# Optimization experiments

Hardware: AMD Instinct MI355X
Metric: run time of the kernel (lower is better)

The kernel has to match this reference:

```python
import jax, jax.numpy as jnp
import numpy as np

K = 49        # k_neighbors
EPS = 1e-5    # BatchNorm2d eps


def setup_inputs() -> dict:
    key = jax.random.key(0)
    ks = jax.random.split(key, 2)
    B, C, M, O = 64, 64, 32, 128
    X = jax.random.normal(ks[0], (B, C, M, M), dtype=jnp.float32)
    # conv1x1 weight (kaiming fan_out) flattened to (O, C); bias init 0
    W = jax.random.normal(ks[1], (O, C), dtype=jnp.float32) * (2.0 / O) ** 0.5
    b = jnp.zeros((O,), jnp.float32)
    gamma = jnp.ones((O,), jnp.float32)
    beta = jnp.zeros((O,), jnp.float32)
    run_mean = jnp.zeros((O,), jnp.float32)
    run_var = jnp.ones((O,), jnp.float32)
    return dict(X=X, W=W, b=b, gamma=gamma, beta=beta,
                run_mean=run_mean, run_var=run_var)


def _knn_aggregate(x):
    """x: (N, C) node features -> D^{-1/2} A D^{-1/2} x for the kNN graph."""
    N = x.shape[0]
    sq = jnp.sum(x * x, axis=1)
    d2 = sq[:, None] + sq[None, :] - 2.0 * (x @ x.T)
    dist = jnp.sqrt(jnp.maximum(d2, 0.0))              # torch.cdist (p=2)
    i = jnp.arange(N)
    dist = dist.at[i, i].set(jnp.inf)                  # fill_diagonal_(inf)
    _, knn = jax.lax.top_k(-dist, K)                   # (N, K) nearest indices
    # topk indices are distinct -> every row degree == K, and the column
    # normalizer uses the col node's row degree (also K), so
    # D^{-1/2} A D^{-1/2} x == mean of gathered neighbors.
    nb = x[knn]                                        # (N, K, C) gather
    return nb.sum(axis=1) / K


def reference(X, W, b, gamma, beta, run_mean, run_var):
    B, C, M, _ = X.shape
    N = M * M
    x = X.reshape(B, C, N).transpose(0, 2, 1)          # (B, N, C) nodes
    Z = jax.vmap(_knn_aggregate)(x)                    # (B, N, C) sparse GCN agg
    # 1x1 conv over the (M, M) grid == per-node linear map
    Fg = jnp.einsum('oc,bnc->bon', W, Z) + b[None, :, None]   # (B, O, N)
    Fg = jax.nn.relu(Fg)
    # BatchNorm2d with running stats (eval mode); Dropout2d is identity in eval
    inv = jax.lax.rsqrt(run_var + EPS)
    Fg = gamma[None, :, None] * (Fg - run_mean[None, :, None]) * inv[None, :, None] + beta[None, :, None]
    return Fg.mean(axis=2)                             # AdaptiveAvgPool2d(1) -> (B, O)
```

## Files before the change

### kernel.cpp

```cpp
#include <hip/hip_runtime.h>
#include <stdint.h>

#define BATCH 64
#define CDIM  64
#define NPTS  1024
#define ODIM  128
#define KNN   49
#define KNNP  52
#define BNEPS 1e-5f

typedef __attribute__((ext_vector_type(8))) short bf16x8;
typedef __attribute__((ext_vector_type(4))) float f32x4;

#define O_XF   0
#define SZ_XF  (BATCH*64*2*64*8*4)
#define O_SQ   (O_XF + SZ_XF)
#define SZ_SQ  (BATCH*NPTS*4)
#define O_KNN  (O_SQ + SZ_SQ)
#define SZ_KNN (BATCH*NPTS*KNNP*4)
#define O_Z    (O_KNN + SZ_KNN)
#define SZ_Z   (BATCH*NPTS*CDIM*4)
#define WS_NEED ((size_t)(O_Z + SZ_Z))

__global__ void gcn_init(const float* __restrict__ gamma, const float* __restrict__ beta,
                         const float* __restrict__ rmean, const float* __restrict__ rvar,
                         float* __restrict__ out) {
    int i = blockIdx.x * 256 + threadIdx.x;
    if (i < BATCH * ODIM) {
        int o = i & (ODIM - 1);
        out[i] = beta[o] - gamma[o] * rmean[o] * rsqrtf(rvar[o] + BNEPS);
    }
}

__global__ __launch_bounds__(256) void k0_split(const float* __restrict__ X,
                                                uint32_t* __restrict__ XF,
                                                float* __restrict__ sq) {
    const int b    = blockIdx.x >> 4;
    const int t16  = (blockIdx.x & 15) * 4 + (threadIdx.x >> 6);
    const int lane = threadIdx.x & 63;
    const int n    = t16 * 16 + (lane & 15);
    const int cg   = lane >> 4;
    const float* Xb = X + (size_t)b * CDIM * NPTS;
    float s = 0.f;
    for (int ks = 0; ks < 2; ks++) {
        uint32_t hi[4], lo[4];
#pragma unroll
        for (int dj = 0; dj < 4; dj++) {
            uint32_t hw[2], lw[2];
#pragma unroll
            for (int e = 0; e < 2; e++) {
                int c = ks * 32 + cg * 8 + dj * 2 + e;
                float x = Xb[(size_t)c * NPTS + n];
                s += x * x;
                uint32_t u  = __float_as_uint(x);
                uint32_t hr = (u + 0x7FFFu + ((u >> 16) & 1u)) >> 16;
                float    hf = __uint_as_float(hr << 16);
                uint32_t ul = __float_as_uint(x - hf);
                uint32_t lr = (ul + 0x7FFFu + ((ul >> 16) & 1u)) >> 16;
                hw[e] = hr; lw[e] = lr;
            }
            hi[dj] = hw[0] | (hw[1] << 16);
            lo[dj] = lw[0] | (lw[1] << 16);
        }
        size_t entry = ((size_t)(b * 64 + t16) * 2 + ks) * 64 + lane;
        uint32_t* p = XF + entry * 8;
        *(uint4*)p       = make_uint4(hi[0], hi[1], hi[2], hi[3]);
        *(uint4*)(p + 4) = make_uint4(lo[0], lo[1], lo[2], lo[3]);
    }
    s += __shfl_xor(s, 16, 64);
    s += __shfl_xor(s, 32, 64);
    if (lane < 16) sq[b * NPTS + n] = s;
}

__global__ __launch_bounds__(512, 6) void k1_gram_select(const uint32_t* __restrict__ XF,
                                                         const float* __restrict__ sq,
                                                         int* __restrict__ knn) {
    __shared__ uint32_t s_pk[8 * 1024];
    const int b    = blockIdx.x >> 6;
    const int rt   = blockIdx.x & 63;
    const int wave = threadIdx.x >> 6, lane = threadIdx.x & 63;
    const int q = lane >> 4, l15 = lane & 15;

    bf16x8 ahi[2], alo[2];
#pragma unroll
    for (int ks = 0; ks < 2; ks++) {
        const uint32_t* p = XF + (((size_t)(b * 64 + rt) * 2 + ks) * 64 + lane) * 8;
        ahi[ks] = *(const bf16x8*)p;
        alo[ks] = *(const bf16x8*)(p + 4);
    }
    const float* sqb = sq + b * NPTS;

#pragma unroll
    for (int tt = 0; tt < 8; tt++) {
        const int t16 = wave * 8 + tt;
        f32x4 acc = {0.f, 0.f, 0.f, 0.f};
#pragma unroll
        for (int ks = 0; ks < 2; ks++) {
            const uint32_t* p = XF + (((size_t)(b * 64 + t16) * 2 + ks) * 64 + lane) * 8;
            bf16x8 bhi = *(const bf16x8*)p;
            bf16x8 blo = *(const bf16x8*)(p + 4);
            acc = __builtin_amdgcn_mfma_f32_16x16x32_bf16(ahi[ks], bhi, acc, 0, 0, 0);
            acc = __builtin_amdgcn_mfma_f32_16x16x32_bf16(alo[ks], bhi, acc, 0, 0, 0);
            acc = __builtin_amdgcn_mfma_f32_16x16x32_bf16(ahi[ks], blo, acc, 0, 0, 0);
        }
        const int col  = t16 * 16 + l15;
        const float sqv = sqb[col];
        uint32_t k16[4];
#pragma unroll
        for (int i = 0; i < 4; i++) {
            int row = q * 4 + i;
            float d = sqv - 2.f * acc[i];
            if (col == rt * 16 + row) d = __uint_as_float(0x7F800000u);
            uint32_t u = __float_as_uint(d);
            uint32_t key = ((int)u < 0) ? ~u : (u | 0x80000000u);
            k16[i] = key >> 16;
        }
        const int p0 = 2 * q, p1 = 2 * q + 1;
        s_pk[p0 * 1024 + (col ^ ((p0 & 3) << 3))] = k16[0] | (k16[1] << 16);
        s_pk[p1 * 1024 + (col ^ ((p1 & 3) << 3))] = k16[2] | (k16[3] << 16);
    }
    __syncthreads();

    uint32_t k0r[16], k1r[16];
    {
        const int sw = (wave & 3) << 3;
#pragma unroll
        for (int tt = 0; tt < 16; tt++) {
            uint32_t pk = s_pk[wave * 1024 + ((tt * 64 + lane) ^ sw)];
            k0r[tt] = pk & 0xFFFFu;
            k1r[tt] = pk >> 16;
        }
    }

    uint32_t lo0, hi0, lo1, hi1;
    {
        uint32_t lm0 = k0r[0], lm1 = k1r[0];
#pragma unroll
        for (int tt = 1; tt < 16; tt++) {
            lm0 = k0r[tt] < lm0 ? k0r[tt] : lm0;
            lm1 = k1r[tt] < lm1 ? k1r[tt] : lm1;
        }
        uint32_t g0 = lm0, m0 = lm0, g1 = lm1, m1 = lm1;
#pragma unroll
        for (int off = 1; off < 64; off <<= 1) {
            uint32_t a0 = (uint32_t)__shfl_xor((int)g0, off, 64);
            uint32_t b0 = (uint32_t)__shfl_xor((int)m0, off, 64);
            uint32_t a1 = (uint32_t)__shfl_xor((int)g1, off, 64);
            uint32_t b1 = (uint32_t)__shfl_xor((int)m1, off, 64);
            g0 = a0 < g0 ? a0 : g0;  m0 = b0 > m0 ? b0 : m0;
            g1 = a1 < g1 ? a1 : g1;  m1 = b1 > m1 ? b1 : m1;
        }
        lo0 = g0; hi0 = m0;
        lo1 = g1; hi1 = m1;
    }

    for (int it = 0; it < 16; it++) {
        bool a0 = lo0 < hi0, a1 = lo1 < hi1;
        if (!a0 && !a1) break;
        uint32_t mid0 = (lo0 + hi0) >> 1;
        uint32_t mid1 = (lo1 + hi1) >> 1;
        int cnt0 = 0, cnt1 = 0;
#pragma unroll
        for (int tt = 0; tt < 16; tt++) {
            cnt0 += __popcll(__ballot(k0r[tt] <= mid0));
            cnt1 += __popcll(__ballot(k1r[tt] <= mid1));
        }
        if (a0) { if (cnt0 >= KNN) hi0 = mid0; else lo0 = mid0 + 1; }
        if (a1) { if (cnt1 >= KNN) hi1 = mid1; else lo1 = mid1 + 1; }
    }

    const unsigned long long ltmask = (1ull << lane) - 1ull;
#pragma unroll
    for (int r = 0; r < 2; r++) {
        const int row = wave * 2 + r;
        const uint32_t vstar = r ? lo1 : lo0;
        const uint32_t* k = r ? k1r : k0r;
        int cntless = 0;
#pragma unroll
        for (int tt = 0; tt < 16; tt++)
            cntless += __popcll(__ballot(k[tt] < vstar));
        const int need = KNN - cntless;
        int base = 0, eqtaken = 0;
        int* kout = knn + ((size_t)b * NPTS + rt * 16 + row) * KNNP;
#pragma unroll
        for (int tt = 0; tt < 16; tt++) {
            bool islt = k[tt] < vstar, iseq = k[tt] == vstar;
            unsigned long long meq = __ballot(iseq);
            int eqrank = eqtaken + __popcll(meq & ltmask);
            bool sel = islt || (iseq && eqrank < need);
            unsigned long long msel = __ballot(sel);
            if (sel) kout[base + __popcll(msel & ltmask)] = tt * 64 + lane;
            base    += __popcll(msel);
            eqtaken += __popcll(meq);
        }
    }
}

__global__ __launch_bounds__(256) void k2a_aggregate(const float* __restrict__ X,
                                                     const int* __restrict__ knn,
                                                     float* __restrict__ z) {
    __shared__ float XT[16 * 1024];
    const int b = blockIdx.x >> 3, cg = (blockIdx.x >> 1) & 3, half = blockIdx.x & 1;
    const int t = threadIdx.x;
    const float* Xb = X + ((size_t)b * CDIM + cg * 16) * NPTS;
#pragma unroll
    for (int nn = 0; nn < 4; nn++) {
        int n = nn * 256 + t;
#pragma unroll
        for (int g = 0; g < 4; g++) {
            float4 v;
            v.x = Xb[(size_t)(4 * g + 0) * NPTS + n];
            v.y = Xb[(size_t)(4 * g + 1) * NPTS + n];
            v.z = Xb[(size_t)(4 * g + 2) * NPTS + n];
            v.w = Xb[(size_t)(4 * g + 3) * NPTS + n];
            int qp = g ^ ((n >> 1) & 3);
            *(float4*)&XT[n * 16 + qp * 4] = v;
        }
    }
    __syncthreads();
    const int wave = t >> 6, lane = t & 63;
    const int r2 = lane >> 4, kb = (lane >> 2) & 3, g = lane & 3;
    for (int rr = 0; rr < 32; rr++) {
        const int row = half * 512 + wave * 128 + rr * 4 + r2;
        const int* kr = knn + ((size_t)b * NPTS + row) * KNNP;
        float4 s = {0.f, 0.f, 0.f, 0.f};
#pragma unroll
        for (int cs = 0; cs < 3; cs++) {
            int4 j4 = *(const int4*)&kr[(kb + 4 * cs) * 4];
            int js[4] = {j4.x, j4.y, j4.z, j4.w};
#pragma unroll
            for (int e = 0; e < 4; e++) {
                int j = js[e];
                float4 v = *(const float4*)&XT[j * 16 + ((g ^ ((j >> 1) & 3)) << 2)];
                s.x += v.x; s.y += v.y; s.z += v.z; s.w += v.w;
            }
        }
        if (kb == 0) {
            int j = kr[48];
            float4 v = *(const float4*)&XT[j * 16 + ((g ^ ((j >> 1) & 3)) << 2)];
            s.x += v.x; s.y += v.y; s.z += v.z; s.w += v.w;
        }
#pragma unroll
        for (int off = 4; off <= 8; off <<= 1) {
            s.x += __shfl_xor(s.x, off, 64);
            s.y += __shfl_xor(s.y, off, 64);
            s.z += __shfl_xor(s.z, off, 64);
            s.w += __shfl_xor(s.w, off, 64);
        }
        if (kb == 0)
            *(float4*)&z[((size_t)b * NPTS + row) * CDIM + cg * 16 + g * 4] = s;
    }
}

__global__ __launch_bounds__(256) void k2b_gemm(const float* __restrict__ z,
                                                const float* __restrict__ W,
                                                const float* __restrict__ bias,
                                                const float* __restrict__ gamma,
                                                const float* __restrict__ rvar,
                                                float* __restrict__ out) {
    __shared__ __align__(16) float s_zz[128 * 64];
    __shared__ float s_red[2][256];
    const int b = blockIdx.x >> 3, nq = blockIdx.x & 7;
    const int t = threadIdx.x;
    const float* zb = z + ((size_t)b * NPTS + nq * 128) * CDIM;
#pragma unroll
    for (int qq = 0; qq < 8; qq++) {
        int e = qq * 256 + t;
        *(float4*)&s_zz[e * 4] = *(const float4*)&zb[e * 4];
    }
    __syncthreads();
    const int o2 = t & 63, h = t >> 6;
    float4 w0[16], w1[16];
#pragma unroll
    for (int c4 = 0; c4 < 16; c4++) {
        w0[c4] = *(const float4*)&W[(size_t)o2 * CDIM + c4 * 4];
        w1[c4] = *(const float4*)&W[(size_t)(o2 + 64) * CDIM + c4 * 4];
    }
    const float b0 = bias[o2], b1 = bias[o2 + 64];
    float r0 = 0.f, r1 = 0.f;
    for (int r = 0; r < 32; r++) {
        const float* zr = &s_zz[(h * 32 + r) * 64];
        float a0 = 0.f, a1 = 0.f;
#pragma unroll
        for (int c4 = 0; c4 < 16; c4++) {
            float4 zv = *(const float4*)&zr[c4 * 4];
            a0 += w0[c4].x * zv.x + w0[c4].y * zv.y + w0[c4].z * zv.z + w0[c4].w * zv.w;
            a1 += w1[c4].x * zv.x + w1[c4].y * zv.y + w1[c4].z * zv.z + w1[c4].w * zv.w;
        }
        r0 += fmaxf(a0 * (1.f / KNN) + b0, 0.f);
        r1 += fmaxf(a1 * (1.f / KNN) + b1, 0.f);
    }
    s_red[0][t] = r0; s_red[1][t] = r1;
    __syncthreads();
    if (t < 128) {
        const int oo = t & 63, which = t >> 6;
        const int o = which * 64 + oo;
        float sum = s_red[which][oo] + s_red[which][64 + oo] +
                    s_red[which][128 + oo] + s_red[which][192 + oo];
        float scale = gamma[o] * rsqrtf(rvar[o] + BNEPS) * (1.f / NPTS);
        atomicAdd(&out[b * ODIM + o], sum * scale);
    }
}

#define RTILE 8
#define APAD  1028
#define WPAD  132
#define POOLF (64 * WPAD)

__global__ __launch_bounds__(256) void gcn_main(
    const float* __restrict__ X, const float* __restrict__ W,
    const float* __restrict__ bias, const float* __restrict__ gamma,
    const float* __restrict__ rvar, float* __restrict__ out)
{
    __shared__ __align__(16) float s_pool[POOLF];
    __shared__ __align__(16) float s_fstage[4][APAD];
    __shared__ int   s_knn[RTILE][KNN];
    __shared__ float s_z[RTILE][CDIM];

    const int t = threadIdx.x;
    const int b = blockIdx.x >> 7;
    const int rtile = blockIdx.x & 127;
    const int r0 = rtile * RTILE;
    const float* Xb = X + (size_t)b * CDIM * NPTS;

    float acc[RTILE][4];
    float sqv[4];
#pragma unroll
    for (int r = 0; r < RTILE; r++)
#pragma unroll
        for (int u = 0; u < 4; u++) acc[r][u] = 0.f;
#pragma unroll
    for (int u = 0; u < 4; u++) sqv[u] = 0.f;

    for (int ch = 0; ch < 16; ch++) {
        const int c0 = ch * 4;
#pragma unroll
        for (int cc = 0; cc < 4; cc++) {
            float4 v = *(const float4*)(Xb + (size_t)(c0 + cc) * NPTS + 4 * t);
            *(float4*)&s_fstage[cc][4 * t] = v;
        }
        __syncthreads();
#pragma unroll
        for (int cc = 0; cc < 4; cc++) {
            float4 bv4 = *(const float4*)&s_fstage[cc][4 * t];
            float bv[4] = {bv4.x, bv4.y, bv4.z, bv4.w};
#pragma unroll
            for (int u = 0; u < 4; u++) sqv[u] += bv[u] * bv[u];
            const float* arow = Xb + (size_t)(c0 + cc) * NPTS + r0;
            float4 a0 = *(const float4*)(arow);
            float4 a1 = *(const float4*)(arow + 4);
            float av[8] = {a0.x, a0.y, a0.z, a0.w, a1.x, a1.y, a1.z, a1.w};
#pragma unroll
            for (int r = 0; r < RTILE; r++)
#pragma unroll
                for (int u = 0; u < 4; u++) acc[r][u] += av[r] * bv[u];
        }
        __syncthreads();
    }

    float* s_dist = s_pool;
#pragma unroll
    for (int r = 0; r < RTILE; r++) {
        const int rG = r0 + r;
        float d[4];
#pragma unroll
        for (int u = 0; u < 4; u++) {
            float dd = sqv[u] - 2.f * acc[r][u];
            d[u] = (4 * t + u == rG) ? __uint_as_float(0x7F800000u) : dd;
        }
        *(float4*)&s_dist[r * NPTS + 4 * t] = make_float4(d[0], d[1], d[2], d[3]);
    }
    __syncthreads();

    const int wave = t >> 6, lane = t & 63;
    const unsigned long long ltmask = (1ull << lane) - 1ull;
    for (int rr = 0; rr < 2; rr++) {
        const int row = wave * 2 + rr;
        unsigned key[16];
#pragma unroll
        for (int tt = 0; tt < 16; tt++) {
            unsigned u = __float_as_uint(s_dist[row * NPTS + tt * 64 + lane]);
            key[tt] = (u & 0x80000000u) ? ~u : (u | 0x80000000u);
        }
        unsigned lo = 0u, hi = 0xFFFFFFFFu;
        while (lo < hi) {
            unsigned mid = lo + ((hi - lo) >> 1);
            int cnt = 0;
#pragma unroll
            for (int tt = 0; tt < 16; tt++)
                cnt += __popcll(__ballot(key[tt] <= mid));
            if (cnt >= KNN) hi = mid; else lo = mid + 1;
        }
        const unsigned v49 = lo;
        int cntless = 0;
#pragma unroll
        for (int tt = 0; tt < 16; tt++)
            cntless += __popcll(__ballot(key[tt] < v49));
        const int need = KNN - cntless;
        int base = 0, eqtaken = 0;
#pragma unroll
        for (int tt = 0; tt < 16; tt++) {
            bool islt = key[tt] < v49;
            bool iseq = key[tt] == v49;
            unsigned long long meq = __ballot(iseq);
            int eqrank = eqtaken + __popcll(meq & ltmask);
            bool sel = islt || (iseq && (eqrank < need));
            unsigned long long msel = __ballot(sel);
            if (sel) {
                int pos = base + __popcll(msel & ltmask);
                s_knn[row][pos] = tt * 64 + lane;
            }
            base    += __popcll(msel);
            eqtaken += __popcll(meq);
        }
    }
    __syncthreads();

    float* astage = s_pool;
    float* s_redf = (float*)s_fstage;
    const int ar = t >> 5, acc8 = (t & 31) >> 2, ks = t & 3;
    for (int c0 = 0; c0 < CDIM; c0 += 8) {
#pragma unroll
        for (int qq = 0; qq < 8; qq++) {
            int if4 = qq * 256 + t;
            int cc = if4 >> 8, j4 = if4 & 255;
            float4 v = *(const float4*)(Xb + (size_t)(c0 + cc) * NPTS + 4 * j4);
            *(float4*)&astage[cc * APAD + 4 * j4] = v;
        }
        __syncthreads();
        float partial = 0.f;
        for (int k = ks; k < KNN; k += 4)
            partial += astage[acc8 * APAD + s_knn[ar][k]];
        s_redf[t] = partial;
        __syncthreads();
        if (t < 64) {
            int r = t >> 3, cc = t & 7;
            int bi = r * 32 + cc * 4;
            s_z[r][c0 + cc] = s_redf[bi] + s_redf[bi + 1] + s_redf[bi + 2] + s_redf[bi + 3];
        }
        __syncthreads();
    }

    float* wt = s_pool;
#pragma unroll 4
    for (int qq = 0; qq < 32; qq++) {
        int e = qq * 256 + t;
        int o = e >> 6, c = e & 63;
        wt[c * WPAD + o] = W[e];
    }
    __syncthreads();
    const int o = t & 127, rg = t >> 7;
    float facc[4] = {0.f, 0.f, 0.f, 0.f};
    for (int c = 0; c < CDIM; c += 4) {
        float w0 = wt[(c + 0) * WPAD + o], w1 = wt[(c + 1) * WPAD + o];
        float w2 = wt[(c + 2) * WPAD + o], w3 = wt[(c + 3) * WPAD + o];
#pragma unroll
        for (int qq = 0; qq < 4; qq++) {
            float4 zv = *(const float4*)&s_z[rg * 4 + qq][c];
            facc[qq] += w0 * zv.x + w1 * zv.y + w2 * zv.z + w3 * zv.w;
        }
    }
    const float bo = bias[o];
    float rsum = 0.f;
#pragma unroll
    for (int qq = 0; qq < 4; qq++) {
        float f = facc[qq] * (1.f / KNN) + bo;
        rsum += fmaxf(f, 0.f);
    }
    s_redf[t] = rsum;
    __syncthreads();
    if (t < 128) {
        float scale = gamma[t] * rsqrtf(rvar[t] + BNEPS) * (1.f / NPTS);
        atomicAdd(&out[b * ODIM + t], (s_redf[t] + s_redf[t + 128]) * scale);
    }
}

extern "C" void kernel_launch(void* const* d_in, const int* in_sizes, int n_in,
                              void* d_out, int out_size, void* d_ws, size_t ws_size,
                              hipStream_t stream) {
    const float* X     = (const float*)d_in[0];
    const float* W     = (const float*)d_in[1];
    const float* bias  = (const float*)d_in[2];
    const float* gamma = (const float*)d_in[3];
    const float* beta  = (const float*)d_in[4];
    const float* rmean = (const float*)d_in[5];
    const float* rvar  = (const float*)d_in[6];
    float* out = (float*)d_out;

    gcn_init<<<(BATCH * ODIM + 255) / 256, 256, 0, stream>>>(gamma, beta, rmean, rvar, out);
    if (ws_size >= WS_NEED) {
        uint8_t* ws = (uint8_t*)d_ws;
        uint32_t* XF  = (uint32_t*)(ws + O_XF);
        float*    sqw = (float*)(ws + O_SQ);
        int*      knn = (int*)(ws + O_KNN);
        float*    zw  = (float*)(ws + O_Z);
        k0_split<<<BATCH * 16, 256, 0, stream>>>(X, XF, sqw);
        k1_gram_select<<<BATCH * 64, 512, 0, stream>>>(XF, sqw, knn);
        k2a_aggregate<<<BATCH * 8, 256, 0, stream>>>(X, knn, zw);
        k2b_gemm<<<BATCH * 8, 256, 0, stream>>>(zw, W, bias, gamma, rvar, out);
    } else {
        gcn_main<<<BATCH * (NPTS / RTILE), 256, 0, stream>>>(X, W, bias, gamma, rvar, out);
    }
}
```

Baseline: 285.5 us.

## Fuse output init into split kernel, simplify kNN emit, one row per lane-quad in aggregate

Folds the output initialisation into the first split kernel, which removes one kernel launch. The kNN index emit now uses separate less-than and equal ballots with mbcnt instead of a third ballot plus a masked popcount. The aggregate kernel assigns a whole row to each group of four lanes, loading all 13 index vectors up front, which drops the cross-lane shuffle reduction. In exchange each lane now issues four times more LDS gathers and holds more registers. A distance computation is also changed to an fma.

```diff
diff --git a/kernel.cpp b/kernel.cpp
--- a/kernel.cpp
+++ b/kernel.cpp
@@ -11,6 +11,11 @@
 
 typedef __attribute__((ext_vector_type(8))) short bf16x8;
 typedef __attribute__((ext_vector_type(4))) float f32x4;
+
+__device__ __forceinline__ int mbcnt64(unsigned long long m) {
+    return __builtin_amdgcn_mbcnt_hi((uint32_t)(m >> 32),
+           __builtin_amdgcn_mbcnt_lo((uint32_t)m, 0));
+}
 
 #define O_XF   0
 #define SZ_XF  (BATCH*64*2*64*8*4)
@@ -34,7 +39,17 @@
 
 __global__ __launch_bounds__(256) void k0_split(const float* __restrict__ X,
                                                 uint32_t* __restrict__ XF,
-                                                float* __restrict__ sq) {
+                                                float* __restrict__ sq,
+                                                const float* __restrict__ gamma,
+                                                const float* __restrict__ beta,
+                                                const float* __restrict__ rmean,
+                                                const float* __restrict__ rvar,
+                                                float* __restrict__ out) {
+    if (blockIdx.x < 32) {
+        int i = blockIdx.x * 256 + threadIdx.x;
+        int o = i & (ODIM - 1);
+        out[i] = beta[o] - gamma[o] * rmean[o] * rsqrtf(rvar[o] + BNEPS);
+    }
     const int b    = blockIdx.x >> 4;
     const int t16  = (blockIdx.x & 15) * 4 + (threadIdx.x >> 6);
     const int lane = threadIdx.x & 63;
@@ -109,7 +124,7 @@
 #pragma unroll
         for (int i = 0; i < 4; i++) {
             int row = q * 4 + i;
-            float d = sqv - 2.f * acc[i];
+            float d = fmaf(-2.f, acc[i], sqv);
             if (col == rt * 16 + row) d = __uint_as_float(0x7F800000u);
             uint32_t u = __float_as_uint(d);
             uint32_t key = ((int)u < 0) ? ~u : (u | 0x80000000u);
@@ -169,29 +184,29 @@
         if (a1) { if (cnt1 >= KNN) hi1 = mid1; else lo1 = mid1 + 1; }
     }
 
-    const unsigned long long ltmask = (1ull << lane) - 1ull;
 #pragma unroll
     for (int r = 0; r < 2; r++) {
         const int row = wave * 2 + r;
         const uint32_t vstar = r ? lo1 : lo0;
         const uint32_t* k = r ? k1r : k0r;
-        int cntless = 0;
+        int total_lt = 0;
 #pragma unroll
         for (int tt = 0; tt < 16; tt++)
-            cntless += __popcll(__ballot(k[tt] < vstar));
-        const int need = KNN - cntless;
-        int base = 0, eqtaken = 0;
+            total_lt += __popcll(__ballot(k[tt] < vstar));
+        int base_lt = 0, base_eq = total_lt;
         int* kout = knn + ((size_t)b * NPTS + rt * 16 + row) * KNNP;
 #pragma unroll
         for (int tt = 0; tt < 16; tt++) {
-            bool islt = k[tt] < vstar, iseq = k[tt] == vstar;
+            bool islt = k[tt] < vstar;
+            bool iseq = k[tt] == vstar;
+            unsigned long long mlt = __ballot(islt);
             unsigned long long meq = __ballot(iseq);
-            int eqrank = eqtaken + __popcll(meq & ltmask);
-            bool sel = islt || (iseq && eqrank < need);
-            unsigned long long msel = __ballot(sel);
-            if (sel) kout[base + __popcll(msel & ltmask)] = tt * 64 + lane;
-            base    += __popcll(msel);
-            eqtaken += __popcll(meq);
+            if (mlt | meq) {
+                int pos = islt ? (base_lt + mbcnt64(mlt)) : (base_eq + mbcnt64(meq));
+                if (islt || (iseq && pos < KNN)) kout[pos] = tt * 64 + lane;
+            }
+            base_lt += __popcll(mlt);
+            base_eq += __popcll(meq);
         }
     }
 }
@@ -219,36 +234,30 @@
     }
     __syncthreads();
     const int wave = t >> 6, lane = t & 63;
-    const int r2 = lane >> 4, kb = (lane >> 2) & 3, g = lane & 3;
-    for (int rr = 0; rr < 32; rr++) {
-        const int row = half * 512 + wave * 128 + rr * 4 + r2;
+    const int rl = lane >> 2, g = lane & 3;
+    for (int rr = 0; rr < 8; rr++) {
+        const int row = half * 512 + wave * 128 + rr * 16 + rl;
         const int* kr = knn + ((size_t)b * NPTS + row) * KNNP;
+        int4 j[13];
+#pragma unroll
+        for (int c = 0; c < 13; c++) j[c] = *(const int4*)&kr[c * 4];
         float4 s = {0.f, 0.f, 0.f, 0.f};
 #pragma unroll
-        for (int cs = 0; cs < 3; cs++) {
-            int4 j4 = *(const int4*)&kr[(kb + 4 * cs) * 4];
-            int js[4] = {j4.x, j4.y, j4.z, j4.w};
+        for (int c = 0; c < 12; c++) {
+            int js[4] = {j[c].x, j[c].y, j[c].z, j[c].w};
 #pragma unroll
             for (int e = 0; e < 4; e++) {
-                int j = js[e];
-                float4 v = *(const float4*)&XT[j * 16 + ((g ^ ((j >> 1) & 3)) << 2)];
+                int jj = js[e];
+                float4 v = *(const float4*)&XT[jj * 16 + ((g ^ ((jj >> 1) & 3)) << 2)];
                 s.x += v.x; s.y += v.y; s.z += v.z; s.w += v.w;
             }
         }
-        if (kb == 0) {
-            int j = kr[48];
-            float4 v = *(const float4*)&XT[j * 16 + ((g ^ ((j >> 1) & 3)) << 2)];
+        {
+            int jj = j[12].x;
+            float4 v = *(const float4*)&XT[jj * 16 + ((g ^ ((jj >> 1) & 3)) << 2)];
             s.x += v.x; s.y += v.y; s.z += v.z; s.w += v.w;
         }
-#pragma unroll
-        for (int off = 4; off <= 8; off <<= 1) {
-            s.x += __shfl_xor(s.x, off, 64);
-            s.y += __shfl_xor(s.y, off, 64);
-            s.z += __shfl_xor(s.z, off, 64);
-            s.w += __shfl_xor(s.w, off, 64);
-        }
-        if (kb == 0)
-            *(float4*)&z[((size_t)b * NPTS + row) * CDIM + cg * 16 + g * 4] = s;
+        *(float4*)&z[((size_t)b * NPTS + row) * CDIM + cg * 16 + g * 4] = s;
     }
 }
 
@@ -487,18 +496,18 @@
     const float* rvar  = (const float*)d_in[6];
     float* out = (float*)d_out;
 
-    gcn_init<<<(BATCH * ODIM + 255) / 256, 256, 0, stream>>>(gamma, beta, rmean, rvar, out);
     if (ws_size >= WS_NEED) {
         uint8_t* ws = (uint8_t*)d_ws;
         uint32_t* XF  = (uint32_t*)(ws + O_XF);
         float*    sqw = (float*)(ws + O_SQ);
         int*      knn = (int*)(ws + O_KNN);
         float*    zw  = (float*)(ws + O_Z);
-        k0_split<<<BATCH * 16, 256, 0, stream>>>(X, XF, sqw);
+        k0_split<<<BATCH * 16, 256, 0, stream>>>(X, XF, sqw, gamma, beta, rmean, rvar, out);
         k1_gram_select<<<BATCH * 64, 512, 0, stream>>>(XF, sqw, knn);
         k2a_aggregate<<<BATCH * 8, 256, 0, stream>>>(X, knn, zw);
         k2b_gemm<<<BATCH * 8, 256, 0, stream>>>(zw, W, bias, gamma, rvar, out);
     } else {
+        gcn_init<<<(BATCH * ODIM + 255) / 256, 256, 0, stream>>>(gamma, beta, rmean, rvar, out);
         gcn_main<<<BATCH * (NPTS / RTILE), 256, 0, stream>>>(X, W, bias, gamma, rvar, out);
     }
 }
```

Result: faster. 273.0 us (-4.4%).
